# Performance work log

Hardware: AMD Instinct MI355X
Metric: run time of the kernel (lower is better)

Reference implementation:

```python
import jax, jax.numpy as jnp
import numpy as np

N, E, D_IN, D_HID, D_OUT, R, B = 50000, 600000, 128, 128, 128, 8, 4


def setup_inputs() -> dict:
    key = jax.random.key(0)
    ks = jax.random.split(key, 12)
    s = 0.05
    return {
        "x": jax.random.normal(ks[0], (N, D_IN), jnp.float32),
        "edge_index": jax.random.randint(ks[1], (2, E), 0, N, jnp.int32),
        "edge_type": jax.random.randint(ks[2], (E,), 0, R, jnp.int32),
        "basis1": jax.random.normal(ks[3], (B, D_IN, D_HID), jnp.float32) * s,
        "comp1": jax.random.normal(ks[4], (R, B), jnp.float32) * s,
        "root1": jax.random.normal(ks[5], (D_IN, D_HID), jnp.float32) * s,
        "bias1": jnp.zeros((D_HID,), jnp.float32),
        "basis2": jax.random.normal(ks[6], (B, D_HID, D_OUT), jnp.float32) * s,
        "comp2": jax.random.normal(ks[7], (R, B), jnp.float32) * s,
        "root2": jax.random.normal(ks[8], (D_HID, D_OUT), jnp.float32) * s,
        "bias2": jnp.zeros((D_OUT,), jnp.float32),
    }


def _rgcn_conv(x, src, dst, etype, basis, comp, root, bias):
    # PyG RGCNConv (basis decomposition, aggr='mean' per relation):
    # out_i = x_i @ root + bias + sum_r mean_{e: type=r, dst=i} (x_src_e @ W_r)
    # W_r linear => aggregate raw features per (node, relation), then transform.
    n = x.shape[0]
    r = comp.shape[0]
    W = jnp.einsum('rb,bio->rio', comp, basis)          # [R, in, out]
    seg = dst * r + etype                               # [E] composite key
    agg = jax.ops.segment_sum(x[src], seg, num_segments=n * r)        # [N*R, in]
    cnt = jax.ops.segment_sum(jnp.ones_like(seg, x.dtype), seg, num_segments=n * r)
    mean = (agg / jnp.maximum(cnt, 1.0)[:, None]).reshape(n, r, -1)   # [N, R, in]
    return jnp.einsum('nri,rio->no', mean, W) + x @ root + bias


def reference(x, edge_index, edge_type, basis1, comp1, root1, bias1,
              basis2, comp2, root2, bias2):
    src, dst = edge_index[0], edge_index[1]
    h = _rgcn_conv(x, src, dst, edge_type, basis1, comp1, root1, bias1)
    h = jax.nn.relu(h)
    # dropout p=0.2 is identity in eval mode
    out = _rgcn_conv(h, src, dst, edge_type, basis2, comp2, root2, bias2)
    return out
```

## Files before the change

### kernel.cpp

```cpp
#include <hip/hip_runtime.h>

#define NN 50000
#define NE 600000
#define DD 128
#define RR 8
#define NBASIS 4
#define NR (NN * RR)
#define KTOT 640
#define MPAD 50048

typedef float f32x4 __attribute__((ext_vector_type(4)));
typedef short bf16x8 __attribute__((ext_vector_type(8)));

static __device__ __forceinline__ unsigned short f2b(float f) {
  union { float f; unsigned u; } c; c.f = f;
  unsigned u = c.u + 0x7fffu + ((c.u >> 16) & 1u);
  return (unsigned short)(u >> 16);
}
static __device__ __forceinline__ unsigned pack2(float lo, float hi) {
  return (unsigned)f2b(lo) | ((unsigned)f2b(hi) << 16);
}
static __device__ __forceinline__ float b2f_lo(unsigned v) {
  union { unsigned u; float f; } c; c.u = v << 16; return c.f;
}
static __device__ __forceinline__ float b2f_hi(unsigned v) {
  union { unsigned u; float f; } c; c.u = v & 0xffff0000u; return c.f;
}

#define PREP_XB 12500
#define PREP_BT 320
#define PREP_CNT 2344
#define PREP_TOTAL (PREP_XB + 2 * PREP_BT + PREP_CNT)

__global__ __launch_bounds__(256) void prep_kernel(
    const float* __restrict__ x, const float* __restrict__ basis1,
    const float* __restrict__ root1, const float* __restrict__ basis2,
    const float* __restrict__ root2, const int* __restrict__ dst,
    const int* __restrict__ et, unsigned* __restrict__ xb,
    unsigned short* __restrict__ BT1, unsigned short* __restrict__ BT2,
    int* __restrict__ cnt) {
  int bid = blockIdx.x;
  int t = threadIdx.x;
  if (bid < PREP_XB) {
    int i = bid * 256 + t;
    float2 v = ((const float2*)x)[i];
    xb[i] = pack2(v.x, v.y);
  } else if (bid < PREP_XB + PREP_BT) {
    int idx = (bid - PREP_XB) * 256 + t;
    int c = idx / KTOT, k = idx - c * KTOT;
    float v = (k < 512) ? basis1[(size_t)((k >> 7) * DD + (k & 127)) * DD + c]
                        : root1[(size_t)(k - 512) * DD + c];
    BT1[idx] = f2b(v);
  } else if (bid < PREP_XB + 2 * PREP_BT) {
    int idx = (bid - PREP_XB - PREP_BT) * 256 + t;
    int c = idx / KTOT, k = idx - c * KTOT;
    float v = (k < 512) ? basis2[(size_t)((k >> 7) * DD + (k & 127)) * DD + c]
                        : root2[(size_t)(k - 512) * DD + c];
    BT2[idx] = f2b(v);
  } else {
    int e = (bid - PREP_XB - 2 * PREP_BT) * 256 + t;
    if (e < NE) atomicAdd(&cnt[dst[e] * RR + et[e]], 1);
  }
}

__global__ __launch_bounds__(256) void offs_kernel(
    const int* __restrict__ cnt, int2* __restrict__ od,
    int* __restrict__ curs, int* __restrict__ gcur) {
  __shared__ int s[256];
  __shared__ int base;
  int t = threadIdx.x;
  int i = blockIdx.x * 256 + t;
  int v = 0;
  if (i < NN) {
    const int4* c4 = (const int4*)cnt;
    int4 a = c4[i * 2];
    int4 b = c4[i * 2 + 1];
    v = a.x + a.y + a.z + a.w + b.x + b.y + b.z + b.w;
  }
  s[t] = v;
  __syncthreads();
  for (int off = 1; off < 256; off <<= 1) {
    int add = (t >= off) ? s[t - off] : 0;
    __syncthreads();
    s[t] += add;
    __syncthreads();
  }
  if (t == 255) base = atomicAdd(gcur, s[255]);
  __syncthreads();
  if (i < NN) {
    int o = base + s[t] - v;
    od[i] = make_int2(o, v);
    curs[i] = o;
  }
}

__global__ __launch_bounds__(256) void sort_kernel(
    const int* __restrict__ src, const int* __restrict__ dst,
    const int* __restrict__ et, int* __restrict__ curs,
    int* __restrict__ skey) {
  int e = blockIdx.x * 256 + threadIdx.x;
  if (e >= NE) return;
  int p = atomicAdd(&curs[dst[e]], 1);
  skey[p] = src[e] | (et[e] << 28);
}

__global__ __launch_bounds__(256) void agg_kernel(
    const uint4* __restrict__ featb4,
    const int* __restrict__ skey, const int* __restrict__ cnt,
    const float* __restrict__ comp, const int2* __restrict__ od,
    uint4* __restrict__ Ab4) {
  __shared__ float ccl[4][RR * NBASIS];
  int tid = threadIdx.x;
  int w = tid >> 6;
  int lane = tid & 63;
  int node = blockIdx.x * 4 + w;
  int g = lane >> 4;
  int q = lane & 15;

  int2 o_d = od[node];
  int beg = o_d.x, dg = o_d.y;

  if (lane < RR * NBASIS) {
    int c = cnt[node * RR + (lane >> 2)];
    ccl[w][lane] = comp[lane] * (1.0f / (float)max(c, 1));
  }
  __syncthreads();

  float a0[8] = {}, a1[8] = {}, a2[8] = {}, a3[8] = {};

  int last = beg + dg - 1;
  const float4* cc4 = (const float4*)ccl[w];
  for (int i = g; i < dg; i += 16) {
    int p0 = beg + i;
    int p1 = min(p0 + 4, last);
    int p2 = min(p0 + 8, last);
    int p3 = min(p0 + 12, last);
    int k0 = skey[p0], k1 = skey[p1], k2 = skey[p2], k3 = skey[p3];
    uint4 v0 = featb4[(size_t)(k0 & 0x0FFFFFFF) * 16 + q];
    uint4 v1 = featb4[(size_t)(k1 & 0x0FFFFFFF) * 16 + q];
    uint4 v2 = featb4[(size_t)(k2 & 0x0FFFFFFF) * 16 + q];
    uint4 v3 = featb4[(size_t)(k3 & 0x0FFFFFFF) * 16 + q];
    float s1 = (i + 4 < dg) ? 1.f : 0.f;
    float s2 = (i + 8 < dg) ? 1.f : 0.f;
    float s3 = (i + 12 < dg) ? 1.f : 0.f;
    float4 c0 = cc4[((unsigned)k0) >> 28];
    float4 c1 = cc4[((unsigned)k1) >> 28];
    float4 c2 = cc4[((unsigned)k2) >> 28];
    float4 c3 = cc4[((unsigned)k3) >> 28];
    c1.x *= s1; c1.y *= s1; c1.z *= s1; c1.w *= s1;
    c2.x *= s2; c2.y *= s2; c2.z *= s2; c2.w *= s2;
    c3.x *= s3; c3.y *= s3; c3.z *= s3; c3.w *= s3;

    float e[8], f[8];
    e[0] = b2f_lo(v0.x); e[1] = b2f_hi(v0.x);
    e[2] = b2f_lo(v0.y); e[3] = b2f_hi(v0.y);
    e[4] = b2f_lo(v0.z); e[5] = b2f_hi(v0.z);
    e[6] = b2f_lo(v0.w); e[7] = b2f_hi(v0.w);
    f[0] = b2f_lo(v1.x); f[1] = b2f_hi(v1.x);
    f[2] = b2f_lo(v1.y); f[3] = b2f_hi(v1.y);
    f[4] = b2f_lo(v1.z); f[5] = b2f_hi(v1.z);
    f[6] = b2f_lo(v1.w); f[7] = b2f_hi(v1.w);
#pragma unroll
    for (int j = 0; j < 8; ++j) {
      a0[j] += c0.x * e[j] + c1.x * f[j];
      a1[j] += c0.y * e[j] + c1.y * f[j];
      a2[j] += c0.z * e[j] + c1.z * f[j];
      a3[j] += c0.w * e[j] + c1.w * f[j];
    }
    e[0] = b2f_lo(v2.x); e[1] = b2f_hi(v2.x);
    e[2] = b2f_lo(v2.y); e[3] = b2f_hi(v2.y);
    e[4] = b2f_lo(v2.z); e[5] = b2f_hi(v2.z);
    e[6] = b2f_lo(v2.w); e[7] = b2f_hi(v2.w);
    f[0] = b2f_lo(v3.x); f[1] = b2f_hi(v3.x);
    f[2] = b2f_lo(v3.y); f[3] = b2f_hi(v3.y);
    f[4] = b2f_lo(v3.z); f[5] = b2f_hi(v3.z);
    f[6] = b2f_lo(v3.w); f[7] = b2f_hi(v3.w);
#pragma unroll
    for (int j = 0; j < 8; ++j) {
      a0[j] += c2.x * e[j] + c3.x * f[j];
      a1[j] += c2.y * e[j] + c3.y * f[j];
      a2[j] += c2.z * e[j] + c3.z * f[j];
      a3[j] += c2.w * e[j] + c3.w * f[j];
    }
  }

#pragma unroll
  for (int j = 0; j < 8; ++j) {
    a0[j] += __shfl_xor(a0[j], 16); a0[j] += __shfl_xor(a0[j], 32);
    a1[j] += __shfl_xor(a1[j], 16); a1[j] += __shfl_xor(a1[j], 32);
    a2[j] += __shfl_xor(a2[j], 16); a2[j] += __shfl_xor(a2[j], 32);
    a3[j] += __shfl_xor(a3[j], 16); a3[j] += __shfl_xor(a3[j], 32);
  }

  uint4* row = Ab4 + (size_t)node * 80;
  uint4 wv;
  if (g == 0) {
    wv.x = pack2(a0[0], a0[1]); wv.y = pack2(a0[2], a0[3]);
    wv.z = pack2(a0[4], a0[5]); wv.w = pack2(a0[6], a0[7]);
  } else if (g == 1) {
    wv.x = pack2(a1[0], a1[1]); wv.y = pack2(a1[2], a1[3]);
    wv.z = pack2(a1[4], a1[5]); wv.w = pack2(a1[6], a1[7]);
  } else if (g == 2) {
    wv.x = pack2(a2[0], a2[1]); wv.y = pack2(a2[2], a2[3]);
    wv.z = pack2(a2[4], a2[5]); wv.w = pack2(a2[6], a2[7]);
  } else {
    wv.x = pack2(a3[0], a3[1]); wv.y = pack2(a3[2], a3[3]);
    wv.z = pack2(a3[4], a3[5]); wv.w = pack2(a3[6], a3[7]);
  }
  row[g * 16 + q] = wv;
  if (g == 0) row[64 + q] = featb4[(size_t)node * 16 + q];
}

template <int OUT_BF16>
__global__ __launch_bounds__(256) void gemm_mfma(
    const unsigned short* __restrict__ Ab, const unsigned short* __restrict__ BT,
    const float* __restrict__ bias, void* __restrict__ Cout) {
  __shared__ unsigned short As[128][64];
  __shared__ unsigned short Bs[128][64];

  int tid = threadIdx.x;
  int row0 = blockIdx.x * 128;
  int lane = tid & 63;
  int wid = tid >> 6;
  int wr = (wid >> 1) * 64;
  int wc = (wid & 1) * 64;

  f32x4 acc[4][4] = {};

  for (int kt = 0; kt < KTOT; kt += 64) {
#pragma unroll
    for (int i = 0; i < 4; ++i) {
      int off = i * 256 + tid;
      int r = off >> 3;
      int ke = (off & 7) << 3;
      *(uint4*)((unsigned short*)As + (size_t)off * 8) =
          *(const uint4*)(Ab + (size_t)(row0 + r) * KTOT + kt + ke);
      *(uint4*)((unsigned short*)Bs + (size_t)off * 8) =
          *(const uint4*)(BT + (size_t)r * KTOT + kt + ke);
    }
    __syncthreads();

#pragma unroll
    for (int kk = 0; kk < 2; ++kk) {
      int ko = kk * 32 + ((lane >> 4) << 3);
      bf16x8 a[4], b[4];
#pragma unroll
      for (int m = 0; m < 4; ++m)
        a[m] = *(const bf16x8*)&As[wr + m * 16 + (lane & 15)][ko];
#pragma unroll
      for (int n = 0; n < 4; ++n)
        b[n] = *(const bf16x8*)&Bs[wc + n * 16 + (lane & 15)][ko];
#pragma unroll
      for (int m = 0; m < 4; ++m)
#pragma unroll
        for (int n = 0; n < 4; ++n)
          acc[m][n] = __builtin_amdgcn_mfma_f32_16x16x32_bf16(
              a[m], b[n], acc[m][n], 0, 0, 0);
    }
    __syncthreads();
  }

#pragma unroll
  for (int n = 0; n < 4; ++n) {
    int col = wc + n * 16 + (lane & 15);
    float bb = bias[col];
#pragma unroll
    for (int m = 0; m < 4; ++m) {
      f32x4 v = acc[m][n];
#pragma unroll
      for (int j = 0; j < 4; ++j) {
        int row = row0 + wr + m * 16 + ((lane >> 4) << 2) + j;
        if (row < NN) {
          float o = v[j] + bb;
          if (OUT_BF16) {
            o = fmaxf(o, 0.f);
            ((unsigned short*)Cout)[(size_t)row * DD + col] = f2b(o);
          } else {
            ((float*)Cout)[(size_t)row * DD + col] = o;
          }
        }
      }
    }
  }
}

extern "C" void kernel_launch(void* const* d_in, const int* in_sizes, int n_in,
                              void* d_out, int out_size, void* d_ws,
                              size_t ws_size, hipStream_t stream) {
  const float* x      = (const float*)d_in[0];
  const int*   eidx   = (const int*)d_in[1];
  const int*   etype  = (const int*)d_in[2];
  const float* basis1 = (const float*)d_in[3];
  const float* comp1  = (const float*)d_in[4];
  const float* root1  = (const float*)d_in[5];
  const float* bias1  = (const float*)d_in[6];
  const float* basis2 = (const float*)d_in[7];
  const float* comp2  = (const float*)d_in[8];
  const float* root2  = (const float*)d_in[9];
  const float* bias2  = (const float*)d_in[10];
  float* out = (float*)d_out;

  const int* src = eidx;
  const int* dst = eidx + NE;

  unsigned short* Ab  = (unsigned short*)d_ws;
  unsigned short* xb  = Ab + (size_t)MPAD * KTOT;
  unsigned short* hb  = xb + (size_t)NN * DD;
  unsigned short* BT1 = hb + (size_t)NN * DD;
  unsigned short* BT2 = BT1 + (size_t)DD * KTOT;
  int*  skey = (int*)(BT2 + (size_t)DD * KTOT);
  int*  cnt  = skey + NE;
  int*  gcur = cnt + NR;
  int2* od   = (int2*)(gcur + 4);
  int*  curs = (int*)(od + NN);

  const int NB = (NN + 255) / 256;
  const int EB = (NE + 255) / 256;

  hipMemsetAsync(cnt, 0, (size_t)(NR + 4) * sizeof(int), stream);
  prep_kernel<<<PREP_TOTAL, 256, 0, stream>>>(
      x, basis1, root1, basis2, root2, dst, etype, (unsigned*)xb, BT1, BT2,
      cnt);
  offs_kernel<<<NB, 256, 0, stream>>>(cnt, od, curs, gcur);
  sort_kernel<<<EB, 256, 0, stream>>>(src, dst, etype, curs, skey);

  int agg_blocks = NN / 4;
  int gemm_blocks = MPAD / 128;

  agg_kernel<<<agg_blocks, 256, 0, stream>>>((const uint4*)xb, skey, cnt,
                                             comp1, od, (uint4*)Ab);
  gemm_mfma<1><<<gemm_blocks, 256, 0, stream>>>(Ab, BT1, bias1, hb);
  agg_kernel<<<agg_blocks, 256, 0, stream>>>((const uint4*)hb, skey, cnt,
                                             comp2, od, (uint4*)Ab);
  gemm_mfma<0><<<gemm_blocks, 256, 0, stream>>>(Ab, BT2, bias2, out);
}
```

Measured before the change: 242.7 us.

## Drop root-feature copy into A matrix, read features directly in GEMM

The aggregation kernel no longer copies each node's own bf16 features into the A matrix. A is now 512 wide instead of 640, and the GEMM reads the last K tile directly from the feature buffer. This removes a redundant write and read of N×128 bf16 per layer. The edge-gather loop is also halved from four to two neighbours per iteration, which lowers register pressure but exposes less memory-level parallelism. Nontemporal loads and stores are added for the A traffic. The feature buffers are padded to MPAD rows so the GEMM's padded row reads stay in bounds.

```diff
diff --git a/kernel.cpp b/kernel.cpp
--- a/kernel.cpp
+++ b/kernel.cpp
@@ -7,10 +7,12 @@
 #define NBASIS 4
 #define NR (NN * RR)
 #define KTOT 640
+#define KZ 512
 #define MPAD 50048
 
 typedef float f32x4 __attribute__((ext_vector_type(4)));
 typedef short bf16x8 __attribute__((ext_vector_type(8)));
+typedef unsigned int u32x4 __attribute__((ext_vector_type(4)));
 
 static __device__ __forceinline__ unsigned short f2b(float f) {
   union { float f; unsigned u; } c; c.f = f;
@@ -105,10 +107,10 @@
 }
 
 __global__ __launch_bounds__(256) void agg_kernel(
-    const uint4* __restrict__ featb4,
+    const u32x4* __restrict__ featb4,
     const int* __restrict__ skey, const int* __restrict__ cnt,
     const float* __restrict__ comp, const int2* __restrict__ od,
-    uint4* __restrict__ Ab4) {
+    u32x4* __restrict__ Ab4) {
   __shared__ float ccl[4][RR * NBASIS];
   int tid = threadIdx.x;
   int w = tid >> 6;
@@ -127,29 +129,20 @@
   __syncthreads();
 
   float a0[8] = {}, a1[8] = {}, a2[8] = {}, a3[8] = {};
-
-  int last = beg + dg - 1;
   const float4* cc4 = (const float4*)ccl[w];
-  for (int i = g; i < dg; i += 16) {
+
+  for (int i = g; i < dg; i += 8) {
     int p0 = beg + i;
-    int p1 = min(p0 + 4, last);
-    int p2 = min(p0 + 8, last);
-    int p3 = min(p0 + 12, last);
-    int k0 = skey[p0], k1 = skey[p1], k2 = skey[p2], k3 = skey[p3];
-    uint4 v0 = featb4[(size_t)(k0 & 0x0FFFFFFF) * 16 + q];
-    uint4 v1 = featb4[(size_t)(k1 & 0x0FFFFFFF) * 16 + q];
-    uint4 v2 = featb4[(size_t)(k2 & 0x0FFFFFFF) * 16 + q];
-    uint4 v3 = featb4[(size_t)(k3 & 0x0FFFFFFF) * 16 + q];
-    float s1 = (i + 4 < dg) ? 1.f : 0.f;
-    float s2 = (i + 8 < dg) ? 1.f : 0.f;
-    float s3 = (i + 12 < dg) ? 1.f : 0.f;
+    bool has2 = (i + 4) < dg;
+    int p1 = has2 ? p0 + 4 : p0;
+    int k0 = skey[p0];
+    int k1 = skey[p1];
+    u32x4 v0 = featb4[(size_t)(k0 & 0x0FFFFFFF) * 16 + q];
+    u32x4 v1 = featb4[(size_t)(k1 & 0x0FFFFFFF) * 16 + q];
     float4 c0 = cc4[((unsigned)k0) >> 28];
     float4 c1 = cc4[((unsigned)k1) >> 28];
-    float4 c2 = cc4[((unsigned)k2) >> 28];
-    float4 c3 = cc4[((unsigned)k3) >> 28];
+    float s1 = has2 ? 1.f : 0.f;
     c1.x *= s1; c1.y *= s1; c1.z *= s1; c1.w *= s1;
-    c2.x *= s2; c2.y *= s2; c2.z *= s2; c2.w *= s2;
-    c3.x *= s3; c3.y *= s3; c3.z *= s3; c3.w *= s3;
 
     float e[8], f[8];
     e[0] = b2f_lo(v0.x); e[1] = b2f_hi(v0.x);
@@ -167,21 +160,6 @@
       a2[j] += c0.z * e[j] + c1.z * f[j];
       a3[j] += c0.w * e[j] + c1.w * f[j];
     }
-    e[0] = b2f_lo(v2.x); e[1] = b2f_hi(v2.x);
-    e[2] = b2f_lo(v2.y); e[3] = b2f_hi(v2.y);
-    e[4] = b2f_lo(v2.z); e[5] = b2f_hi(v2.z);
-    e[6] = b2f_lo(v2.w); e[7] = b2f_hi(v2.w);
-    f[0] = b2f_lo(v3.x); f[1] = b2f_hi(v3.x);
-    f[2] = b2f_lo(v3.y); f[3] = b2f_hi(v3.y);
-    f[4] = b2f_lo(v3.z); f[5] = b2f_hi(v3.z);
-    f[6] = b2f_lo(v3.w); f[7] = b2f_hi(v3.w);
-#pragma unroll
-    for (int j = 0; j < 8; ++j) {
-      a0[j] += c2.x * e[j] + c3.x * f[j];
-      a1[j] += c2.y * e[j] + c3.y * f[j];
-      a2[j] += c2.z * e[j] + c3.z * f[j];
-      a3[j] += c2.w * e[j] + c3.w * f[j];
-    }
   }
 
 #pragma unroll
@@ -192,8 +170,7 @@
     a3[j] += __shfl_xor(a3[j], 16); a3[j] += __shfl_xor(a3[j], 32);
   }
 
-  uint4* row = Ab4 + (size_t)node * 80;
-  uint4 wv;
+  u32x4 wv;
   if (g == 0) {
     wv.x = pack2(a0[0], a0[1]); wv.y = pack2(a0[2], a0[3]);
     wv.z = pack2(a0[4], a0[5]); wv.w = pack2(a0[6], a0[7]);
@@ -207,13 +184,14 @@
     wv.x = pack2(a3[0], a3[1]); wv.y = pack2(a3[2], a3[3]);
     wv.z = pack2(a3[4], a3[5]); wv.w = pack2(a3[6], a3[7]);
   }
-  row[g * 16 + q] = wv;
-  if (g == 0) row[64 + q] = featb4[(size_t)node * 16 + q];
+  __builtin_nontemporal_store(wv, Ab4 + (size_t)node * 64 + g * 16 + q);
 }
 
 template <int OUT_BF16>
 __global__ __launch_bounds__(256) void gemm_mfma(
-    const unsigned short* __restrict__ Ab, const unsigned short* __restrict__ BT,
+    const unsigned short* __restrict__ Ab,
+    const unsigned short* __restrict__ feat,
+    const unsigned short* __restrict__ BT,
     const float* __restrict__ bias, void* __restrict__ Cout) {
   __shared__ unsigned short As[128][64];
   __shared__ unsigned short Bs[128][64];
@@ -233,10 +211,16 @@
       int off = i * 256 + tid;
       int r = off >> 3;
       int ke = (off & 7) << 3;
-      *(uint4*)((unsigned short*)As + (size_t)off * 8) =
-          *(const uint4*)(Ab + (size_t)(row0 + r) * KTOT + kt + ke);
-      *(uint4*)((unsigned short*)Bs + (size_t)off * 8) =
-          *(const uint4*)(BT + (size_t)r * KTOT + kt + ke);
+      u32x4 av;
+      if (kt < KZ)
+        av = __builtin_nontemporal_load(
+            (const u32x4*)(Ab + (size_t)(row0 + r) * KZ + kt + ke));
+      else
+        av = __builtin_nontemporal_load(
+            (const u32x4*)(feat + (size_t)(row0 + r) * DD + (kt - KZ) + ke));
+      *(u32x4*)((unsigned short*)As + (size_t)off * 8) = av;
+      *(u32x4*)((unsigned short*)Bs + (size_t)off * 8) =
+          *(const u32x4*)(BT + (size_t)r * KTOT + kt + ke);
     }
     __syncthreads();
 
@@ -304,9 +288,9 @@
   const int* dst = eidx + NE;
 
   unsigned short* Ab  = (unsigned short*)d_ws;
-  unsigned short* xb  = Ab + (size_t)MPAD * KTOT;
-  unsigned short* hb  = xb + (size_t)NN * DD;
-  unsigned short* BT1 = hb + (size_t)NN * DD;
+  unsigned short* xb  = Ab + (size_t)MPAD * KZ;
+  unsigned short* hb  = xb + (size_t)MPAD * DD;
+  unsigned short* BT1 = hb + (size_t)MPAD * DD;
   unsigned short* BT2 = BT1 + (size_t)DD * KTOT;
   int*  skey = (int*)(BT2 + (size_t)DD * KTOT);
   int*  cnt  = skey + NE;
@@ -327,10 +311,10 @@
   int agg_blocks = NN / 4;
   int gemm_blocks = MPAD / 128;
 
-  agg_kernel<<<agg_blocks, 256, 0, stream>>>((const uint4*)xb, skey, cnt,
-                                             comp1, od, (uint4*)Ab);
-  gemm_mfma<1><<<gemm_blocks, 256, 0, stream>>>(Ab, BT1, bias1, hb);
-  agg_kernel<<<agg_blocks, 256, 0, stream>>>((const uint4*)hb, skey, cnt,
-                                             comp2, od, (uint4*)Ab);
-  gemm_mfma<0><<<gemm_blocks, 256, 0, stream>>>(Ab, BT2, bias2, out);
-}
+  agg_kernel<<<agg_blocks, 256, 0, stream>>>((const u32x4*)xb, skey, cnt,
+                                             comp1, od, (u32x4*)Ab);
+  gemm_mfma<1><<<gemm_blocks, 256, 0, stream>>>(Ab, xb, BT1, bias1, hb);
+  agg_kernel<<<agg_blocks, 256, 0, stream>>>((const u32x4*)hb, skey, cnt,
+                                             comp2, od, (u32x4*)Ab);
+  gemm_mfma<0><<<gemm_blocks, 256, 0, stream>>>(Ab, hb, BT2, bias2, out);
+}
```

Result: slower. 250.7 us (+3.3%).
